# Kernel optimization log

Measured on AMD Instinct MI355X. Metric: run time of the kernel, lower is better.

Reference implementation:

```python
import jax, jax.numpy as jnp
import numpy as np
from jax import lax

WINDOW_SIZE = 11
SIGMA = 1.5
CHANNEL = 1
C1 = 0.01 ** 2
C2 = 0.03 ** 2


def _gaussian_1d(size, sigma):
    coords = jnp.arange(size, dtype=jnp.float32) - size // 2
    g = jnp.exp(-coords ** 2 / (2.0 * sigma ** 2))
    return g / g.sum()


def create_window_3d(window_size, channel, sigma=SIGMA):
    g = _gaussian_1d(window_size, sigma)
    # outer products -> (ws, ws, ws), normalized 3D Gaussian
    w3 = jnp.einsum('i,j,k->ijk', g, g, g)
    # (channel, 1, ws, ws, ws) for grouped (depthwise) conv, OIDHW layout
    return jnp.broadcast_to(w3[None, None], (channel, 1, window_size, window_size, window_size))


def _conv3d(x, window, channel):
    # padding window_size//2 with odd window == SAME
    return lax.conv_general_dilated(
        x, window,
        window_strides=(1, 1, 1),
        padding='SAME',
        feature_group_count=channel,
        dimension_numbers=('NCDHW', 'OIDHW', 'NCDHW'))


def setup_inputs() -> dict:
    key = jax.random.key(0)
    k1, k2 = jax.random.split(key)
    shape = (4, CHANNEL, 128, 128, 128)
    img1 = jax.random.uniform(k1, shape, dtype=jnp.float32)
    img2 = jax.random.uniform(k2, shape, dtype=jnp.float32)
    window = create_window_3d(WINDOW_SIZE, CHANNEL)
    return {"img1": img1, "img2": img2, "window": window}


def reference(img1, img2, window):
    channel = img1.shape[1]
    mu1 = _conv3d(img1, window, channel)
    mu2 = _conv3d(img2, window, channel)
    mu1_sq = mu1 * mu1
    mu2_sq = mu2 * mu2
    mu1_mu2 = mu1 * mu2
    sigma1_sq = _conv3d(img1 * img1, window, channel) - mu1_sq
    sigma2_sq = _conv3d(img2 * img2, window, channel) - mu2_sq
    sigma12 = _conv3d(img1 * img2, window, channel) - mu1_mu2
    ssim_map = ((2 * mu1_mu2 + C1) * (2 * sigma12 + C2)) / (
        (mu1_sq + mu2_sq + C1) * (sigma1_sq + sigma2_sq + C2))
    return ssim_map.mean()  # size_average=True
```

## Files before the change

### kernel.cpp

```cpp
#include <hip/hip_runtime.h>


#define SLICE (128*128)
#define S  (128*SLICE)
#define ZROW 640
#define ZSL  81920
#define C1_ 0.0001f
#define C2_ 0.0009f

__device__ __forceinline__ void make_g_s(float* gs) {
    float g[11]; float s = 0.f;
#pragma unroll
    for (int i = 0; i < 11; ++i) {
        float d = (float)(i - 5);
        g[i] = __expf(-d * d / 4.5f);
        s += g[i];
    }
    float inv = 1.f / s;
#pragma unroll
    for (int i = 0; i < 11; ++i)
        gs[i] = __int_as_float(__builtin_amdgcn_readfirstlane(
                    __float_as_int(g[i] * inv)));
}

#define RB    160
#define RSLOT (2*RB)
#define WRING (4*RSLOT)

#define STEPA(T_, TM_, J0_, J1_, STORE_, OKC_) do {                           \
    const int T__ = (T_);                                                     \
    int sp__ = T__ + 4; if (sp__ > 25) sp__ = 25;                             \
    int rowc__ = min(max(y0 + sp__ - 5, 0), 127);                             \
    float4 Rn__ = *(const float4*)(src + (size_t)rowc__ * 128);               \
    if (OKC_) {                                                               \
        const float* rp__ = p_rd + ((T_) & 3) * RSLOT;                        \
        float u1__ = 0.f, u2__ = 0.f, a11__ = 0.f, a22__ = 0.f, a12__ = 0.f;  \
        _Pragma("unroll")                                                     \
        for (int j = 0; j < 6; ++j) {                                         \
            float2 va__ = *(const float2*)(rp__ + 2 * j);                     \
            float2 vb__ = *(const float2*)(rp__ + RB + 2 * j);                \
            {                                                                 \
                float wj__ = w12[2 * j];                                      \
                float ta__ = wj__ * va__.x, tb__ = wj__ * vb__.x;             \
                u1__ += ta__; u2__ += tb__;                                   \
                a11__ = fmaf(ta__, va__.x, a11__);                            \
                a12__ = fmaf(ta__, vb__.x, a12__);                            \
                a22__ = fmaf(tb__, vb__.x, a22__);                            \
            }                                                                 \
            {                                                                 \
                float wj__ = w12[2 * j + 1];                                  \
                float ta__ = wj__ * va__.y, tb__ = wj__ * vb__.y;             \
                u1__ += ta__; u2__ += tb__;                                   \
                a11__ = fmaf(ta__, va__.y, a11__);                            \
                a12__ = fmaf(ta__, vb__.y, a12__);                            \
                a22__ = fmaf(tb__, vb__.y, a22__);                            \
            }                                                                 \
        }                                                                     \
        _Pragma("unroll")                                                     \
        for (int j = (J0_); j <= (J1_); ++j) {                                \
            const int sl__ = ((TM_) + j + 1) % 11;                            \
            float wy__ = gs[10 - j];                                          \
            acc[0][sl__] = fmaf(wy__, u1__,  acc[0][sl__]);                   \
            acc[1][sl__] = fmaf(wy__, u2__,  acc[1][sl__]);                   \
            acc[2][sl__] = fmaf(wy__, a11__, acc[2][sl__]);                   \
            acc[3][sl__] = fmaf(wy__, a22__, acc[3][sl__]);                   \
            acc[4][sl__] = fmaf(wy__, a12__, acc[4][sl__]);                   \
        }                                                                     \
    }                                                                         \
    *(float4*)(p_wr + (((T_) + 2) & 3) * RSLOT) = h1;            \
    if (STORE_) {                                                             \
        size_t wo__ = (size_t)(y0 + T__ - 10) * ZROW;                         \
        const int es__ = ((TM_) + 1) % 11;                                    \
        _Pragma("unroll")                                                     \
        for (int f = 0; f < 5; ++f) {                                         \
            fb[wo__ + f * 128] = acc[f][es__];                                \
            acc[f][es__] = 0.f;                                               \
        }                                                                     \
    }                                                                         \
    h1 = h2; h2 = Rn__;                                                       \
} while (0)

__global__ __launch_bounds__(128, 2)
void ssimA(const float* __restrict__ img1, const float* __restrict__ img2,
           float* __restrict__ fields) {
    __shared__ __align__(16) float ring[2 * WRING];
    float gs[11]; make_g_s(gs);
    const int x = threadIdx.x;
    const int w = x >> 6, l = x & 63;
    const int b = blockIdx.x;
    const int yc = b & 7, z = (b >> 3) & 127, n = b >> 10;
    const int y0 = yc * 16;
    const float* src = (l < 32 ? img1 : img2)
                     + (size_t)n * S + (size_t)z * SLICE + 4 * (l & 31);
    float* fb = fields + (size_t)(n * 128 + z) * ZSL + x;

    const int p = (x - 5) & 1;
    const int e = (x - 5) - p;
    float w12[12];
#pragma unroll
    for (int k = 0; k < 12; ++k) {
        float we = (k <= 10) ? gs[k] : 0.f;
        float wo = (k >= 1) ? gs[k - 1] : 0.f;
        w12[k] = p ? wo : we;
    }

    float* wring = ring + w * WRING;
    float* p_rd = wring + (8 + e);
    float* p_wr = wring + ((l < 32) ? 0 : RB) + 8 + 4 * (l & 31);

    for (int i = l; i < WRING; i += 64) wring[i] = 0.f;

    float acc[5][11];
#pragma unroll
    for (int f = 0; f < 5; ++f)
#pragma unroll
        for (int s2 = 0; s2 < 11; ++s2) acc[f][s2] = 0.f;

    float4 h1, h2;
    {
        int r0 = min(max(y0 - 5, 0), 127);
        int r1 = min(max(y0 - 4, 0), 127);
        int r2 = min(max(y0 - 3, 0), 127);
        int r3 = min(max(y0 - 2, 0), 127);
        float4 R0 = *(const float4*)(src + (size_t)r0 * 128);
        float4 R1 = *(const float4*)(src + (size_t)r1 * 128);
        h1        = *(const float4*)(src + (size_t)r2 * 128);
        h2        = *(const float4*)(src + (size_t)r3 * 128);
        *(float4*)(p_wr)         = R0;
        *(float4*)(p_wr + RSLOT) = R1;
    }

#pragma unroll
    for (int t = 0; t < 10; ++t)
        STEPA(t, t, 10 - t, 10, false, (y0 + t - 5 >= 0));
#pragma unroll
    for (int t = 10; t < 16; ++t)
        STEPA(t, t % 11, 0, 10, true, true);
#pragma unroll
    for (int t = 16; t < 26; ++t)
        STEPA(t, t % 11, 0, 25 - t, true, (y0 + t - 5 < 128));
}

#define STEPB(T_, TM_, J0_, J1_, STORE_, OKC_) do {                           \
    const int T__ = (T_);                                                     \
    int sp__ = T__ + 4; if (sp__ > 41) sp__ = 41;                             \
    size_t off__ = (size_t)min(max(z0 + sp__ - 5, 0), 127) * ZSL;             \
    float N0__ = base[off__];                                                 \
    float N1__ = base[off__ + 128];                                           \
    float N2__ = base[off__ + 256];                                           \
    float N3__ = base[off__ + 384];                                           \
    float N4__ = base[off__ + 512];                                           \
    if (OKC_) {                                                               \
        _Pragma("unroll")                                                     \
        for (int j = (J0_); j <= (J1_); ++j) {                                \
            const int sl__ = ((TM_) + j + 1) % 11;                            \
            float wz__ = gs[10 - j];                                          \
            acc[0][sl__] = fmaf(wz__, P0[0], acc[0][sl__]);                   \
            acc[1][sl__] = fmaf(wz__, P0[1], acc[1][sl__]);                   \
            acc[2][sl__] = fmaf(wz__, P0[2], acc[2][sl__]);                   \
            acc[3][sl__] = fmaf(wz__, P0[3], acc[3][sl__]);                   \
            acc[4][sl__] = fmaf(wz__, P0[4], acc[4][sl__]);                   \
        }                                                                     \
    }                                                                         \
    if (STORE_) {                                                             \
        const int es__ = ((TM_) + 1) % 11;                                    \
        float m1__ = acc[0][es__], m2__ = acc[1][es__];                       \
        float p11__ = acc[2][es__], p22__ = acc[3][es__], p12__ = acc[4][es__];\
        float m1s__ = m1__ * m1__, m2s__ = m2__ * m2__, m12__ = m1__ * m2__;  \
        float v1c__ = p11__ - m1s__, v2c__ = p22__ - m2s__, cv__ = p12__ - m12__;\
        float num__ = (2.f * m12__ + C1_) * (2.f * cv__ + C2_);               \
        float den__ = (m1s__ + m2s__ + C1_) * (v1c__ + v2c__ + C2_);          \
        sum += num__ / den__;                                                 \
        _Pragma("unroll")                                                     \
        for (int f = 0; f < 5; ++f) acc[f][es__] = 0.f;                       \
    }                                                                         \
    _Pragma("unroll")                                                         \
    for (int f = 0; f < 5; ++f) { P0[f] = P1[f]; P1[f] = P2[f]; P2[f] = P3[f]; } \
    P3[0] = N0__; P3[1] = N1__; P3[2] = N2__; P3[3] = N3__; P3[4] = N4__;     \
} while (0)

__global__ __launch_bounds__(128, 2)
void ssimB(const float* __restrict__ fields, float* __restrict__ partials) {
    float gs[11]; make_g_s(gs);
    const int tid = threadIdx.x;
    const int x = tid;
    const int b = blockIdx.x;
    const int zc = b & 3, y = (b >> 2) & 127;
    const int n = 3 - (b >> 9);
    const int z0 = zc * 32;
    const float* base = fields + (size_t)n * 128 * ZSL + (size_t)y * ZROW + x;

    float acc[5][11];
#pragma unroll
    for (int f = 0; f < 5; ++f)
#pragma unroll
        for (int s2 = 0; s2 < 11; ++s2) acc[f][s2] = 0.f;

    float sum = 0.f;

    float P0[5], P1[5], P2[5], P3[5];
    {
        size_t o0 = (size_t)min(max(z0 - 5, 0), 127) * ZSL;
        size_t o1 = (size_t)min(max(z0 - 4, 0), 127) * ZSL;
        size_t o2 = (size_t)min(max(z0 - 3, 0), 127) * ZSL;
        size_t o3 = (size_t)min(max(z0 - 2, 0), 127) * ZSL;
#pragma unroll
        for (int f = 0; f < 5; ++f) {
            P0[f] = base[o0 + f * 128];
            P1[f] = base[o1 + f * 128];
            P2[f] = base[o2 + f * 128];
            P3[f] = base[o3 + f * 128];
        }
    }

#pragma unroll
    for (int t = 0; t < 10; ++t)
        STEPB(t, t, 10 - t, 10, false, (z0 + t - 5 >= 0));
#pragma unroll 1
    for (int blk = 0; blk < 2; ++blk) {
#pragma unroll
        for (int tt = 0; tt < 11; ++tt)
            STEPB(10 + blk * 11 + tt, (10 + tt) % 11, 0, 10, true, true);
    }
#pragma unroll
    for (int t = 32; t < 42; ++t)
        STEPB(t, t % 11, 0, 41 - t, true, (z0 + t - 5 < 128));

#pragma unroll
    for (int o = 32; o > 0; o >>= 1) sum += __shfl_down(sum, o, 64);
    __shared__ float ws2[2];
    if ((tid & 63) == 0) ws2[tid >> 6] = sum;
    __syncthreads();
    if (tid == 0) partials[blockIdx.x] = ws2[0] + ws2[1];
}

__global__ void ssim_final(const float* __restrict__ partial, int n,
                           float* __restrict__ out, double inv_count) {
    int tid = threadIdx.x;
    double s = 0.0;
    for (int i = tid; i < n; i += 256) s += (double)partial[i];
#pragma unroll
    for (int o = 32; o > 0; o >>= 1) s += __shfl_down(s, o, 64);
    __shared__ double wsum[4];
    int lane = tid & 63, wid = tid >> 6;
    if (lane == 0) wsum[wid] = s;
    __syncthreads();
    if (tid == 0)
        out[0] = (float)((wsum[0] + wsum[1] + wsum[2] + wsum[3]) * inv_count);
}

extern "C" void kernel_launch(void* const* d_in, const int* in_sizes, int n_in,
                              void* d_out, int out_size, void* d_ws, size_t ws_size,
                              hipStream_t stream) {
    const float* img1 = (const float*)d_in[0];
    const float* img2 = (const float*)d_in[1];
    float* out = (float*)d_out;

    float* fields   = (float*)d_ws;
    float* partials = fields + 20 * (size_t)S;

    ssimA<<<4096, 128, 0, stream>>>(img1, img2, fields);
    ssimB<<<2048, 128, 0, stream>>>(fields, partials);
    ssim_final<<<1, 256, 0, stream>>>(partials, 2048, out,
                                      1.0 / ((double)S * 4));
}
```

Before: 181.4 us.

## Merge the two squared-intensity fields into one and deepen z-prefetch

SSIM only uses sigma1_sq + sigma2_sq, so the blurred img1^2 and img2^2 fields are folded into a single blurred (img1^2 + img2^2) field. This cuts the intermediate field buffer from five to four channels, reducing global writes in the first pass and reads in the second, along with register use for the accumulators. The second pass also prefetches two more z-planes ahead (six staged planes instead of four) to hide load latency better. Summing the squares before subtracting the mean terms slightly changes floating-point rounding.

```diff
diff --git a/kernel.cpp b/kernel.cpp
--- a/kernel.cpp
+++ b/kernel.cpp
@@ -3,8 +3,8 @@
 
 #define SLICE (128*128)
 #define S  (128*SLICE)
-#define ZROW 640
-#define ZSL  81920
+#define ZROW 512
+#define ZSL  65536
 #define C1_ 0.0001f
 #define C2_ 0.0009f
 
@@ -34,7 +34,7 @@
     float4 Rn__ = *(const float4*)(src + (size_t)rowc__ * 128);               \
     if (OKC_) {                                                               \
         const float* rp__ = p_rd + ((T_) & 3) * RSLOT;                        \
-        float u1__ = 0.f, u2__ = 0.f, a11__ = 0.f, a22__ = 0.f, a12__ = 0.f;  \
+        float u1__ = 0.f, u2__ = 0.f, ss__ = 0.f, a12__ = 0.f;                \
         _Pragma("unroll")                                                     \
         for (int j = 0; j < 6; ++j) {                                         \
             float2 va__ = *(const float2*)(rp__ + 2 * j);                     \
@@ -43,17 +43,17 @@
                 float wj__ = w12[2 * j];                                      \
                 float ta__ = wj__ * va__.x, tb__ = wj__ * vb__.x;             \
                 u1__ += ta__; u2__ += tb__;                                   \
-                a11__ = fmaf(ta__, va__.x, a11__);                            \
+                ss__  = fmaf(ta__, va__.x, ss__);                             \
+                ss__  = fmaf(tb__, vb__.x, ss__);                             \
                 a12__ = fmaf(ta__, vb__.x, a12__);                            \
-                a22__ = fmaf(tb__, vb__.x, a22__);                            \
             }                                                                 \
             {                                                                 \
                 float wj__ = w12[2 * j + 1];                                  \
                 float ta__ = wj__ * va__.y, tb__ = wj__ * vb__.y;             \
                 u1__ += ta__; u2__ += tb__;                                   \
-                a11__ = fmaf(ta__, va__.y, a11__);                            \
+                ss__  = fmaf(ta__, va__.y, ss__);                             \
+                ss__  = fmaf(tb__, vb__.y, ss__);                             \
                 a12__ = fmaf(ta__, vb__.y, a12__);                            \
-                a22__ = fmaf(tb__, vb__.y, a22__);                            \
             }                                                                 \
         }                                                                     \
         _Pragma("unroll")                                                     \
@@ -62,9 +62,8 @@
             float wy__ = gs[10 - j];                                          \
             acc[0][sl__] = fmaf(wy__, u1__,  acc[0][sl__]);                   \
             acc[1][sl__] = fmaf(wy__, u2__,  acc[1][sl__]);                   \
-            acc[2][sl__] = fmaf(wy__, a11__, acc[2][sl__]);                   \
-            acc[3][sl__] = fmaf(wy__, a22__, acc[3][sl__]);                   \
-            acc[4][sl__] = fmaf(wy__, a12__, acc[4][sl__]);                   \
+            acc[2][sl__] = fmaf(wy__, ss__,  acc[2][sl__]);                   \
+            acc[3][sl__] = fmaf(wy__, a12__, acc[3][sl__]);                   \
         }                                                                     \
     }                                                                         \
     *(float4*)(p_wr + (((T_) + 2) & 3) * RSLOT) = h1;            \
@@ -72,7 +71,7 @@
         size_t wo__ = (size_t)(y0 + T__ - 10) * ZROW;                         \
         const int es__ = ((TM_) + 1) % 11;                                    \
         _Pragma("unroll")                                                     \
-        for (int f = 0; f < 5; ++f) {                                         \
+        for (int f = 0; f < 4; ++f) {                                         \
             fb[wo__ + f * 128] = acc[f][es__];                                \
             acc[f][es__] = 0.f;                                               \
         }                                                                     \
@@ -110,9 +109,9 @@
 
     for (int i = l; i < WRING; i += 64) wring[i] = 0.f;
 
-    float acc[5][11];
-#pragma unroll
-    for (int f = 0; f < 5; ++f)
+    float acc[4][11];
+#pragma unroll
+    for (int f = 0; f < 4; ++f)
 #pragma unroll
         for (int s2 = 0; s2 < 11; ++s2) acc[f][s2] = 0.f;
 
@@ -143,13 +142,12 @@
 
 #define STEPB(T_, TM_, J0_, J1_, STORE_, OKC_) do {                           \
     const int T__ = (T_);                                                     \
-    int sp__ = T__ + 4; if (sp__ > 41) sp__ = 41;                             \
+    int sp__ = T__ + 6; if (sp__ > 41) sp__ = 41;                             \
     size_t off__ = (size_t)min(max(z0 + sp__ - 5, 0), 127) * ZSL;             \
     float N0__ = base[off__];                                                 \
     float N1__ = base[off__ + 128];                                           \
     float N2__ = base[off__ + 256];                                           \
     float N3__ = base[off__ + 384];                                           \
-    float N4__ = base[off__ + 512];                                           \
     if (OKC_) {                                                               \
         _Pragma("unroll")                                                     \
         for (int j = (J0_); j <= (J1_); ++j) {                                \
@@ -159,24 +157,27 @@
             acc[1][sl__] = fmaf(wz__, P0[1], acc[1][sl__]);                   \
             acc[2][sl__] = fmaf(wz__, P0[2], acc[2][sl__]);                   \
             acc[3][sl__] = fmaf(wz__, P0[3], acc[3][sl__]);                   \
-            acc[4][sl__] = fmaf(wz__, P0[4], acc[4][sl__]);                   \
         }                                                                     \
     }                                                                         \
     if (STORE_) {                                                             \
         const int es__ = ((TM_) + 1) % 11;                                    \
         float m1__ = acc[0][es__], m2__ = acc[1][es__];                       \
-        float p11__ = acc[2][es__], p22__ = acc[3][es__], p12__ = acc[4][es__];\
+        float ps__ = acc[2][es__], p12__ = acc[3][es__];                      \
         float m1s__ = m1__ * m1__, m2s__ = m2__ * m2__, m12__ = m1__ * m2__;  \
-        float v1c__ = p11__ - m1s__, v2c__ = p22__ - m2s__, cv__ = p12__ - m12__;\
+        float v12__ = ps__ - m1s__ - m2s__;          \
+        float cv__  = p12__ - m12__;                             \
         float num__ = (2.f * m12__ + C1_) * (2.f * cv__ + C2_);               \
-        float den__ = (m1s__ + m2s__ + C1_) * (v1c__ + v2c__ + C2_);          \
+        float den__ = (m1s__ + m2s__ + C1_) * (v12__ + C2_);                  \
         sum += num__ / den__;                                                 \
         _Pragma("unroll")                                                     \
-        for (int f = 0; f < 5; ++f) acc[f][es__] = 0.f;                       \
+        for (int f = 0; f < 4; ++f) acc[f][es__] = 0.f;                       \
     }                                                                         \
     _Pragma("unroll")                                                         \
-    for (int f = 0; f < 5; ++f) { P0[f] = P1[f]; P1[f] = P2[f]; P2[f] = P3[f]; } \
-    P3[0] = N0__; P3[1] = N1__; P3[2] = N2__; P3[3] = N3__; P3[4] = N4__;     \
+    for (int f = 0; f < 4; ++f) {                                             \
+        P0[f] = P1[f]; P1[f] = P2[f]; P2[f] = P3[f];                          \
+        P3[f] = P4[f]; P4[f] = P5[f];                                         \
+    }                                                                         \
+    P5[0] = N0__; P5[1] = N1__; P5[2] = N2__; P5[3] = N3__;                   \
 } while (0)
 
 __global__ __launch_bounds__(128, 2)
@@ -190,26 +191,30 @@
     const int z0 = zc * 32;
     const float* base = fields + (size_t)n * 128 * ZSL + (size_t)y * ZROW + x;
 
-    float acc[5][11];
-#pragma unroll
-    for (int f = 0; f < 5; ++f)
+    float acc[4][11];
+#pragma unroll
+    for (int f = 0; f < 4; ++f)
 #pragma unroll
         for (int s2 = 0; s2 < 11; ++s2) acc[f][s2] = 0.f;
 
     float sum = 0.f;
 
-    float P0[5], P1[5], P2[5], P3[5];
+    float P0[4], P1[4], P2[4], P3[4], P4[4], P5[4];
     {
         size_t o0 = (size_t)min(max(z0 - 5, 0), 127) * ZSL;
         size_t o1 = (size_t)min(max(z0 - 4, 0), 127) * ZSL;
         size_t o2 = (size_t)min(max(z0 - 3, 0), 127) * ZSL;
         size_t o3 = (size_t)min(max(z0 - 2, 0), 127) * ZSL;
-#pragma unroll
-        for (int f = 0; f < 5; ++f) {
+        size_t o4 = (size_t)min(max(z0 - 1, 0), 127) * ZSL;
+        size_t o5 = (size_t)min(max(z0 - 0, 0), 127) * ZSL;
+#pragma unroll
+        for (int f = 0; f < 4; ++f) {
             P0[f] = base[o0 + f * 128];
             P1[f] = base[o1 + f * 128];
             P2[f] = base[o2 + f * 128];
             P3[f] = base[o3 + f * 128];
+            P4[f] = base[o4 + f * 128];
+            P5[f] = base[o5 + f * 128];
         }
     }
 
@@ -257,7 +262,7 @@
     float* out = (float*)d_out;
 
     float* fields   = (float*)d_ws;
-    float* partials = fields + 20 * (size_t)S;
+    float* partials = fields + 16 * (size_t)S;
 
     ssimA<<<4096, 128, 0, stream>>>(img1, img2, fields);
     ssimB<<<2048, 128, 0, stream>>>(fields, partials);
```

Result: faster. 176.2 us (-2.9%).
